# Kernel optimization log

Hardware: AMD Instinct MI355X
Metric: run time of the kernel (lower is better)

The kernel has to match this reference:

```python
import jax, jax.numpy as jnp
import numpy as np

NUM_PROTOTYPES = 512
NUM_BLOCKS = 8
D_MODEL = 1024
D_BLOCK = D_MODEL // NUM_BLOCKS


def setup_inputs() -> dict:
    key = jax.random.key(0)
    kq, km = jax.random.split(key)
    queries = jax.random.normal(kq, (8, 1024, D_MODEL), dtype=jnp.float32)
    # learned codebook: nn.Embedding(num_blocks*num_prototypes, d_block), normal init
    mem = jax.random.normal(km, (NUM_BLOCKS * NUM_PROTOTYPES, D_BLOCK), dtype=jnp.float32)
    return {"queries": queries, "mem": mem}


def reference(queries, mem):
    B, N, _ = queries.shape
    m, p, d = NUM_BLOCKS, NUM_PROTOTYPES, D_BLOCK
    q = queries.reshape(B, N, m, d)                 # [B,N,m,d]
    codes = mem.reshape(m, p, d)                    # [m,p,d]
    # Squared distances restricted to each query's own block (the only entries
    # the original consumes via distances[i, :, i]):
    #   ||q||^2 - 2 q.c + ||c||^2
    dots = jnp.einsum('bnmd,mpd->bnmp', q, codes)   # [B,N,m,p]
    qn = jnp.sum(q * q, axis=-1)                    # [B,N,m]
    cn = jnp.sum(codes * codes, axis=-1)            # [m,p]
    dist = qn[..., None] - 2.0 * dots + cn[None, None]
    local = jnp.argmin(dist, axis=-1)               # [B,N,m], first-min tiebreak like torch max of -dist
    indices = local + jnp.arange(m, dtype=local.dtype)[None, None, :] * p
    emb = codes[jnp.arange(m)[None, None, :], local]          # [B,N,m,d]
    emb = emb.reshape(B, N, m * d)
    # straight-through estimator
    emb_st = jax.lax.stop_gradient(emb - queries) + queries
    vq_loss = jnp.asarray(0.0, dtype=queries.dtype)
    commitment_loss = jnp.mean((jax.lax.stop_gradient(emb) - queries) ** 2)
    return emb_st, indices, vq_loss, commitment_loss
```

## Files before the change

### kernel.cpp

```cpp
#include <hip/hip_runtime.h>

#define NPROTO 512
#define NBLK 8
#define DB 128
#define DM 1024

#define IDX_OFF  8388608
#define VQ_OFF   8454144
#define CL_OFF   8454145

typedef unsigned short u16;
typedef __attribute__((ext_vector_type(8))) _Float16 f16x8;
typedef __attribute__((ext_vector_type(16))) float f32x16;

#define BH_B   0u
#define BL_B   1048576u
#define CN_B   2097152u
#define PART_B 2113536u
#define WS_NEED (PART_B + 16384u)

__global__ __launch_bounds__(256) void vq_prep(const float* __restrict__ src,
                                               u16* __restrict__ hi,
                                               u16* __restrict__ lo,
                                               float* __restrict__ cn) {
    const int t  = threadIdx.x;
    const int p  = blockIdx.x * 32 + (t >> 3);
    const int g  = t & 7;
    const int m  = p >> 9, pm = p & 511;
    const float* s = src + (size_t)p * DB + g * 16;
    float sq = 0.f;
    ushort4 h[4], l[4];
    #pragma unroll
    for (int j = 0; j < 4; ++j) {
        float4 v = *(const float4*)(s + j * 4);
        float x; _Float16 hf;
        #define S1(c, f) x = v.c; hf = (_Float16)x; h[j].f = __builtin_bit_cast(u16, hf); \
            hf = (_Float16)(x - (float)hf); l[j].f = __builtin_bit_cast(u16, hf); sq += x * x;
        S1(x, x) S1(y, y) S1(z, z) S1(w, w)
        #undef S1
    }
    const size_t o0 = ((size_t)((m * 8 + g) * 2 + 0) * 512 + pm) * 8;
    const size_t o1 = ((size_t)((m * 8 + g) * 2 + 1) * 512 + pm) * 8;
    *(uint4*)(hi + o0) = *(uint4*)&h[0];
    *(uint4*)(hi + o1) = *(uint4*)&h[2];
    *(uint4*)(lo + o0) = *(uint4*)&l[0];
    *(uint4*)(lo + o1) = *(uint4*)&l[2];
    sq += __shfl_xor(sq, 1, 64);
    sq += __shfl_xor(sq, 2, 64);
    sq += __shfl_xor(sq, 4, 64);
    if ((t & 7) == 0) cn[p] = sq;
}

__device__ __forceinline__ unsigned cvt2(float x, float y, unsigned& lo) {
    _Float16 hx = (_Float16)x, hy = (_Float16)y;
    _Float16 lx = (_Float16)(x - (float)hx), ly = (_Float16)(y - (float)hy);
    lo = (unsigned)__builtin_bit_cast(u16, lx) | ((unsigned)__builtin_bit_cast(u16, ly) << 16);
    return (unsigned)__builtin_bit_cast(u16, hx) | ((unsigned)__builtin_bit_cast(u16, hy) << 16);
}

__global__ __launch_bounds__(256, 2) void vq_fused(
        const float* __restrict__ q, const float* __restrict__ mem,
        const u16* __restrict__ bh, const u16* __restrict__ bl,
        const float* __restrict__ cn, float* __restrict__ out,
        float* __restrict__ partials2) {
    __shared__ __align__(16) u16 Ap[4][2][8][66][8];
    __shared__ float qn_lds[128];
    __shared__ int   bp[128];

    const int t    = threadIdx.x;
    const int lane = t & 63;
    const int w    = t >> 6;
    const int col  = lane & 31;
    const int kg   = lane >> 5;
    const int m    = blockIdx.y;
    const int bn0  = blockIdx.x * 128;
    const int rbase = w * 32;

    {
        const int row = lane >> 1;
        const int hf  = lane & 1;
        const float* src = q + (size_t)(bn0 + rbase + row) * DM + m * DB + hf * 64;
        float sq = 0.f;
        #pragma unroll
        for (int k4 = 0; k4 < 4; ++k4) {
            const int kst = hf * 4 + k4;
            float4 v0 = ((const float4*)(src + k4 * 16))[0];
            float4 v1 = ((const float4*)(src + k4 * 16))[1];
            float4 v2 = ((const float4*)(src + k4 * 16))[2];
            float4 v3 = ((const float4*)(src + k4 * 16))[3];
            sq += v0.x*v0.x+v0.y*v0.y+v0.z*v0.z+v0.w*v0.w
                + v1.x*v1.x+v1.y*v1.y+v1.z*v1.z+v1.w*v1.w
                + v2.x*v2.x+v2.y*v2.y+v2.z*v2.z+v2.w*v2.w
                + v3.x*v3.x+v3.y*v3.y+v3.z*v3.z+v3.w*v3.w;
            unsigned l0,l1,l2,l3,l4,l5,l6,l7;
            unsigned h0 = cvt2(v0.x, v0.y, l0), h1 = cvt2(v0.z, v0.w, l1);
            unsigned h2 = cvt2(v1.x, v1.y, l2), h3 = cvt2(v1.z, v1.w, l3);
            unsigned h4 = cvt2(v2.x, v2.y, l4), h5 = cvt2(v2.z, v2.w, l5);
            unsigned h6 = cvt2(v3.x, v3.y, l6), h7 = cvt2(v3.z, v3.w, l7);
            *(uint4*)&Ap[w][0][kst][row][0]      = make_uint4(h0, h1, h2, h3);
            *(uint4*)&Ap[w][0][kst][row + 32][0] = make_uint4(h4, h5, h6, h7);
            *(uint4*)&Ap[w][1][kst][row][0]      = make_uint4(l0, l1, l2, l3);
            *(uint4*)&Ap[w][1][kst][row + 32][0] = make_uint4(l4, l5, l6, l7);
        }
        sq += __shfl_xor(sq, 1, 64);
        if (hf == 0) qn_lds[rbase + row] = sq;
    }

    const u16* bh_l = bh + ((size_t)(m * 16 + kg) * 512 + col) * 8;
    const u16* bl_l = bl + ((size_t)(m * 16 + kg) * 512 + col) * 8;

    float bestv[16]; int besti[16];
    #pragma unroll
    for (int r = 0; r < 16; ++r) { bestv[r] = 3.4e38f; besti[r] = 0; }

    #pragma unroll 2
    for (int c = 0; c < 16; ++c) {
        const float cnv = cn[m * NPROTO + c * 32 + col];
        const u16* bhc = bh_l + c * 256;
        const u16* blc = bl_l + c * 256;
        f32x16 aA, aB;
        #pragma unroll
        for (int r = 0; r < 16; ++r) { aA[r] = 0.f; aB[r] = 0.f; }
        #pragma unroll
        for (int kst = 0; kst < 8; ++kst) {
            f16x8 Bh = *(const f16x8*)(bhc + kst * 8192);
            f16x8 Bl = *(const f16x8*)(blc + kst * 8192);
            f16x8 Ah = *(const f16x8*)&Ap[w][0][kst][lane][0];
            f16x8 Al = *(const f16x8*)&Ap[w][1][kst][lane][0];
            aA = __builtin_amdgcn_mfma_f32_32x32x16_f16(Ah, Bh, aA, 0, 0, 0);
            aB = __builtin_amdgcn_mfma_f32_32x32x16_f16(Al, Bh, aB, 0, 0, 0);
            aB = __builtin_amdgcn_mfma_f32_32x32x16_f16(Ah, Bl, aB, 0, 0, 0);
        }
        const int ix = c * 32 + col;
        #pragma unroll
        for (int r = 0; r < 16; ++r) {
            float d = cnv - 2.0f * (aA[r] + aB[r]);
            if (d < bestv[r]) { bestv[r] = d; besti[r] = ix; }
        }
    }

    #pragma unroll
    for (int r = 0; r < 16; ++r) {
        float v = bestv[r]; int ix = besti[r];
        #pragma unroll
        for (int off = 1; off < 32; off <<= 1) {
            float v2 = __shfl_xor(v, off, 64);
            int  ix2 = __shfl_xor(ix, off, 64);
            if (v2 < v || (v2 == v && ix2 < ix)) { v = v2; ix = ix2; }
        }
        bestv[r] = v; besti[r] = ix;
    }

    if (col == 0) {
        float lp = 0.f;
        #pragma unroll
        for (int r = 0; r < 16; ++r) {
            int row = rbase + (r & 3) + 8 * (r >> 2) + 4 * kg;
            bp[row] = besti[r];
            out[(size_t)IDX_OFF + (size_t)(bn0 + row) * NBLK + m] =
                (float)(m * NPROTO + besti[r]);
            lp += bestv[r] + qn_lds[row];
        }
        partials2[((size_t)blockIdx.y * gridDim.x + blockIdx.x) * 8 + w * 2 + kg] = lp;
    }

    {
        const int row = lane >> 1, hf = lane & 1;
        const int bpi = bp[rbase + row];
        const float* cv = mem + ((size_t)(m * NPROTO + bpi)) * DB + hf * 64;
        float* ov = out + (size_t)(bn0 + rbase + row) * DM + m * DB + hf * 64;
        #pragma unroll
        for (int j = 0; j < 16; ++j)
            ((float4*)ov)[j] = ((const float4*)cv)[j];
    }
}

__global__ __launch_bounds__(256) void vq_init(const float* __restrict__ mem,
                                               float* __restrict__ cn) {
    int p = blockIdx.x * 256 + threadIdx.x;
    const float* c = mem + (size_t)p * DB;
    float s = 0.f;
    #pragma unroll 8
    for (int k = 0; k < DB; k += 4) {
        float4 v = *(const float4*)(c + k);
        s += v.x * v.x + v.y * v.y + v.z * v.z + v.w * v.w;
    }
    cn[p] = s;
}

__global__ __launch_bounds__(256, 1) void vq_main_f32(const float* __restrict__ q,
                                                      const float* __restrict__ mem,
                                                      const float* __restrict__ cn,
                                                      float* __restrict__ out,
                                                      float* __restrict__ partials) {
    __shared__ float q_lds[128 * 132];
    __shared__ float c_lds[128 * 132];
    __shared__ float red[256];

    const int t    = threadIdx.x;
    const int tile = blockIdx.x;
    const int m    = blockIdx.y;
    const int tr   = t >> 4;
    const int tc   = t & 15;
    const int bn0  = tile * 128;

    const float* qbase = q + (size_t)bn0 * DM + m * DB;
    #pragma unroll
    for (int it = 0; it < 16; ++it) {
        int idx = it * 256 + t;
        int row = idx >> 5;
        int c4  = (idx & 31) << 2;
        *(float4*)&q_lds[row * 132 + c4] = *(const float4*)(qbase + (size_t)row * DM + c4);
    }

    float bestv[8]; int besti[8];
    #pragma unroll
    for (int i = 0; i < 8; ++i) { bestv[i] = 3.4e38f; besti[i] = 0; }
    const float* cbase = mem + (size_t)m * NPROTO * DB;

    for (int ch = 0; ch < 4; ++ch) {
        __syncthreads();
        const float* cb = cbase + (size_t)ch * 128 * DB;
        #pragma unroll
        for (int it = 0; it < 16; ++it) {
            int idx = it * 256 + t;
            int row = idx >> 5;
            int c4  = (idx & 31) << 2;
            *(float4*)&c_lds[row * 132 + c4] = *(const float4*)(cb + row * DB + c4);
        }
        __syncthreads();

        float acc[8][8];
        #pragma unroll
        for (int i = 0; i < 8; ++i)
            #pragma unroll
            for (int j = 0; j < 8; ++j) acc[i][j] = 0.f;

        for (int d4 = 0; d4 < DB; d4 += 4) {
            float4 qa[8], cvv[8];
            #pragma unroll
            for (int i = 0; i < 8; ++i) qa[i] = *(const float4*)&q_lds[(tr + 16 * i) * 132 + d4];
            #pragma unroll
            for (int j = 0; j < 8; ++j) cvv[j] = *(const float4*)&c_lds[(tc + 16 * j) * 132 + d4];
            #pragma unroll
            for (int i = 0; i < 8; ++i)
                #pragma unroll
                for (int j = 0; j < 8; ++j) {
                    acc[i][j] += qa[i].x * cvv[j].x; acc[i][j] += qa[i].y * cvv[j].y;
                    acc[i][j] += qa[i].z * cvv[j].z; acc[i][j] += qa[i].w * cvv[j].w;
                }
        }
        #pragma unroll
        for (int i = 0; i < 8; ++i)
            #pragma unroll
            for (int j = 0; j < 8; ++j) {
                int lp = ch * 128 + tc + 16 * j;
                float dist = cn[m * NPROTO + lp] - 2.0f * acc[i][j];
                if (dist < bestv[i]) { bestv[i] = dist; besti[i] = lp; }
            }
    }

    #pragma unroll
    for (int i = 0; i < 8; ++i) {
        float v = bestv[i]; int ix = besti[i];
        #pragma unroll
        for (int off = 1; off < 16; off <<= 1) {
            float v2 = __shfl_xor(v, off, 64);
            int  ix2 = __shfl_xor(ix, off, 64);
            if (v2 < v || (v2 == v && ix2 < ix)) { v = v2; ix = ix2; }
        }
        bestv[i] = v; besti[i] = ix;
    }

    float lacc = 0.f;
    #pragma unroll
    for (int i = 0; i < 8; ++i) {
        int row = tr + 16 * i;
        int bn  = bn0 + row;
        const float* cvec = cbase + (size_t)besti[i] * DB;
        float* orow = out + (size_t)bn * DM + m * DB;
        #pragma unroll
        for (int h = 0; h < 2; ++h) {
            int colx = h * 64 + tc * 4;
            float4 c4v = *(const float4*)(cvec + colx);
            *(float4*)(orow + colx) = c4v;
            float4 qv2 = *(const float4*)&q_lds[row * 132 + colx];
            float dx = c4v.x - qv2.x, dy = c4v.y - qv2.y;
            float dz = c4v.z - qv2.z, dw = c4v.w - qv2.w;
            lacc += dx * dx + dy * dy + dz * dz + dw * dw;
        }
        if (tc == 0)
            out[(size_t)IDX_OFF + (size_t)bn * NBLK + m] = (float)(m * NPROTO + besti[i]);
    }

    red[t] = lacc;
    __syncthreads();
    for (int s = 128; s > 0; s >>= 1) {
        if (t < s) red[t] += red[t + s];
        __syncthreads();
    }
    if (t == 0) partials[blockIdx.y * gridDim.x + blockIdx.x] = red[0];
}

__global__ __launch_bounds__(256) void vq_final(const float* __restrict__ partials,
                                                float* __restrict__ out, int n) {
    __shared__ float red[256];
    int t = threadIdx.x;
    float v = 0.f;
    for (int i = t; i < n; i += 256) v += partials[i];
    red[t] = v;
    __syncthreads();
    for (int s = 128; s > 0; s >>= 1) {
        if (t < s) red[t] += red[t + s];
        __syncthreads();
    }
    if (t == 0) {
        out[VQ_OFF] = 0.f;
        out[CL_OFF] = red[0] / 8388608.0f;
    }
}

extern "C" void kernel_launch(void* const* d_in, const int* in_sizes, int n_in,
                              void* d_out, int out_size, void* d_ws, size_t ws_size,
                              hipStream_t stream) {
    const float* q   = (const float*)d_in[0];
    const float* mem = (const float*)d_in[1];
    float* out = (float*)d_out;
    char* ws = (char*)d_ws;

    if (ws_size >= (size_t)WS_NEED) {
        u16*   bhp = (u16*)(ws + BH_B);
        u16*   blp = (u16*)(ws + BL_B);
        float* cnp = (float*)(ws + CN_B);
        float* partials = (float*)(ws + PART_B);

        vq_prep<<<128, 256, 0, stream>>>(mem, bhp, blp, cnp);
        dim3 grid(64, 8);
        vq_fused<<<grid, 256, 0, stream>>>(q, mem, bhp, blp, cnp, out, partials);
        vq_final<<<1, 256, 0, stream>>>(partials, out, 4096);
    } else {
        float* cn = (float*)ws;
        float* partials = cn + 4096;
        vq_init<<<16, 256, 0, stream>>>(mem, cn);
        dim3 grid(64, 8);
        vq_main_f32<<<grid, 256, 0, stream>>>(q, mem, cn, out, partials);
        vq_final<<<1, 256, 0, stream>>>(partials, out, 512);
    }
}
```

Baseline: 69.54 us.

## Switch to 16x16x32 MFMA with register-resident A and smaller row tiles

Replaces the 32x32x16 MFMA tiling with 16x16x32 MFMAs, holding each wave's query fragments (fp16 hi/lo split) directly in registers instead of staging them through LDS. Each block now handles 64 rows instead of 128, doubling the grid to 1024 blocks, and the codebook pre-pack layout is changed to match the new K-step grouping. This is meant to remove LDS staging and raise occupancy and parallelism. The cost is that each codebook fragment is reused across fewer query rows, so codebook loads per row roughly double, and there are more partial sums to reduce in the final kernel.

```diff
diff --git a/kernel.cpp b/kernel.cpp
--- a/kernel.cpp
+++ b/kernel.cpp
@@ -11,13 +11,13 @@
 
 typedef unsigned short u16;
 typedef __attribute__((ext_vector_type(8))) _Float16 f16x8;
-typedef __attribute__((ext_vector_type(16))) float f32x16;
+typedef __attribute__((ext_vector_type(4))) float f32x4;
 
 #define BH_B   0u
 #define BL_B   1048576u
 #define CN_B   2097152u
 #define PART_B 2113536u
-#define WS_NEED (PART_B + 16384u)
+#define WS_NEED (PART_B + 65536u)
 
 __global__ __launch_bounds__(256) void vq_prep(const float* __restrict__ src,
                                                u16* __restrict__ hi,
@@ -39,8 +39,9 @@
         S1(x, x) S1(y, y) S1(z, z) S1(w, w)
         #undef S1
     }
-    const size_t o0 = ((size_t)((m * 8 + g) * 2 + 0) * 512 + pm) * 8;
-    const size_t o1 = ((size_t)((m * 8 + g) * 2 + 1) * 512 + pm) * 8;
+    const int kst = g >> 1, kg0 = (g & 1) * 2;
+    const size_t o0 = (((size_t)(m * 4 + kst) * 4 + kg0 + 0) * 512 + pm) * 8;
+    const size_t o1 = (((size_t)(m * 4 + kst) * 4 + kg0 + 1) * 512 + pm) * 8;
     *(uint4*)(hi + o0) = *(uint4*)&h[0];
     *(uint4*)(hi + o1) = *(uint4*)&h[2];
     *(uint4*)(lo + o0) = *(uint4*)&l[0];
@@ -63,87 +64,83 @@
         const u16* __restrict__ bh, const u16* __restrict__ bl,
         const float* __restrict__ cn, float* __restrict__ out,
         float* __restrict__ partials2) {
-    __shared__ __align__(16) u16 Ap[4][2][8][66][8];
-    __shared__ float qn_lds[128];
-    __shared__ int   bp[128];
+    __shared__ float qn_l[64];
+    __shared__ int   bp[64];
 
     const int t    = threadIdx.x;
     const int lane = t & 63;
     const int w    = t >> 6;
-    const int col  = lane & 31;
-    const int kg   = lane >> 5;
+    const int pr   = lane & 15;
+    const int kg   = lane >> 4;
     const int m    = blockIdx.y;
-    const int bn0  = blockIdx.x * 128;
-    const int rbase = w * 32;
-
-    {
-        const int row = lane >> 1;
-        const int hf  = lane & 1;
-        const float* src = q + (size_t)(bn0 + rbase + row) * DM + m * DB + hf * 64;
-        float sq = 0.f;
-        #pragma unroll
-        for (int k4 = 0; k4 < 4; ++k4) {
-            const int kst = hf * 4 + k4;
-            float4 v0 = ((const float4*)(src + k4 * 16))[0];
-            float4 v1 = ((const float4*)(src + k4 * 16))[1];
-            float4 v2 = ((const float4*)(src + k4 * 16))[2];
-            float4 v3 = ((const float4*)(src + k4 * 16))[3];
-            sq += v0.x*v0.x+v0.y*v0.y+v0.z*v0.z+v0.w*v0.w
-                + v1.x*v1.x+v1.y*v1.y+v1.z*v1.z+v1.w*v1.w
-                + v2.x*v2.x+v2.y*v2.y+v2.z*v2.z+v2.w*v2.w
-                + v3.x*v3.x+v3.y*v3.y+v3.z*v3.z+v3.w*v3.w;
-            unsigned l0,l1,l2,l3,l4,l5,l6,l7;
-            unsigned h0 = cvt2(v0.x, v0.y, l0), h1 = cvt2(v0.z, v0.w, l1);
-            unsigned h2 = cvt2(v1.x, v1.y, l2), h3 = cvt2(v1.z, v1.w, l3);
-            unsigned h4 = cvt2(v2.x, v2.y, l4), h5 = cvt2(v2.z, v2.w, l5);
-            unsigned h6 = cvt2(v3.x, v3.y, l6), h7 = cvt2(v3.z, v3.w, l7);
-            *(uint4*)&Ap[w][0][kst][row][0]      = make_uint4(h0, h1, h2, h3);
-            *(uint4*)&Ap[w][0][kst][row + 32][0] = make_uint4(h4, h5, h6, h7);
-            *(uint4*)&Ap[w][1][kst][row][0]      = make_uint4(l0, l1, l2, l3);
-            *(uint4*)&Ap[w][1][kst][row + 32][0] = make_uint4(l4, l5, l6, l7);
-        }
-        sq += __shfl_xor(sq, 1, 64);
-        if (hf == 0) qn_lds[rbase + row] = sq;
-    }
-
-    const u16* bh_l = bh + ((size_t)(m * 16 + kg) * 512 + col) * 8;
-    const u16* bl_l = bl + ((size_t)(m * 16 + kg) * 512 + col) * 8;
-
-    float bestv[16]; int besti[16];
-    #pragma unroll
-    for (int r = 0; r < 16; ++r) { bestv[r] = 3.4e38f; besti[r] = 0; }
+    const int bn0  = blockIdx.x * 64;
+    const int rbase = w * 16;
+
+    f16x8 ah[4], al[4];
+    float qnp = 0.f;
+    #pragma unroll
+    for (int kst = 0; kst < 4; ++kst) {
+        const float* src = q + (size_t)(bn0 + rbase + pr) * DM
+                             + m * DB + kst * 32 + kg * 8;
+        float4 v0 = ((const float4*)src)[0];
+        float4 v1 = ((const float4*)src)[1];
+        unsigned l0, l1, l2, l3;
+        unsigned h0 = cvt2(v0.x, v0.y, l0), h1 = cvt2(v0.z, v0.w, l1);
+        unsigned h2 = cvt2(v1.x, v1.y, l2), h3 = cvt2(v1.z, v1.w, l3);
+        uint4 hv = make_uint4(h0, h1, h2, h3), lv = make_uint4(l0, l1, l2, l3);
+        ah[kst] = __builtin_bit_cast(f16x8, hv);
+        al[kst] = __builtin_bit_cast(f16x8, lv);
+        qnp += v0.x*v0.x + v0.y*v0.y + v0.z*v0.z + v0.w*v0.w
+             + v1.x*v1.x + v1.y*v1.y + v1.z*v1.z + v1.w*v1.w;
+    }
+    qnp += __shfl_xor(qnp, 16, 64);
+    qnp += __shfl_xor(qnp, 32, 64);
+    if (kg == 0) qn_l[rbase + pr] = qnp;
+
+    const u16* bh_l = bh + ((size_t)(m * 16 + kg) * 512 + pr) * 8;
+    const u16* bl_l = bl + ((size_t)(m * 16 + kg) * 512 + pr) * 8;
+    const float* cnb = cn + m * NPROTO + pr;
+
+    float bestv[4]; int besti[4];
+    #pragma unroll
+    for (int r = 0; r < 4; ++r) { bestv[r] = 3.4e38f; besti[r] = 0; }
 
     #pragma unroll 2
     for (int c = 0; c < 16; ++c) {
-        const float cnv = cn[m * NPROTO + c * 32 + col];
+        const float cn0 = cnb[c * 32];
+        const float cn1 = cnb[c * 32 + 16];
         const u16* bhc = bh_l + c * 256;
         const u16* blc = bl_l + c * 256;
-        f32x16 aA, aB;
-        #pragma unroll
-        for (int r = 0; r < 16; ++r) { aA[r] = 0.f; aB[r] = 0.f; }
-        #pragma unroll
-        for (int kst = 0; kst < 8; ++kst) {
-            f16x8 Bh = *(const f16x8*)(bhc + kst * 8192);
-            f16x8 Bl = *(const f16x8*)(blc + kst * 8192);
-            f16x8 Ah = *(const f16x8*)&Ap[w][0][kst][lane][0];
-            f16x8 Al = *(const f16x8*)&Ap[w][1][kst][lane][0];
-            aA = __builtin_amdgcn_mfma_f32_32x32x16_f16(Ah, Bh, aA, 0, 0, 0);
-            aB = __builtin_amdgcn_mfma_f32_32x32x16_f16(Al, Bh, aB, 0, 0, 0);
-            aB = __builtin_amdgcn_mfma_f32_32x32x16_f16(Ah, Bl, aB, 0, 0, 0);
-        }
-        const int ix = c * 32 + col;
-        #pragma unroll
-        for (int r = 0; r < 16; ++r) {
-            float d = cnv - 2.0f * (aA[r] + aB[r]);
-            if (d < bestv[r]) { bestv[r] = d; besti[r] = ix; }
-        }
-    }
-
-    #pragma unroll
-    for (int r = 0; r < 16; ++r) {
+        f32x4 a0A = {0.f,0.f,0.f,0.f}, a0B = {0.f,0.f,0.f,0.f};
+        f32x4 a1A = {0.f,0.f,0.f,0.f}, a1B = {0.f,0.f,0.f,0.f};
+        #pragma unroll
+        for (int kst = 0; kst < 4; ++kst) {
+            f16x8 Bh0 = *(const f16x8*)(bhc + (size_t)kst * 16384);
+            f16x8 Bl0 = *(const f16x8*)(blc + (size_t)kst * 16384);
+            f16x8 Bh1 = *(const f16x8*)(bhc + (size_t)kst * 16384 + 128);
+            f16x8 Bl1 = *(const f16x8*)(blc + (size_t)kst * 16384 + 128);
+            a0A = __builtin_amdgcn_mfma_f32_16x16x32_f16(ah[kst], Bh0, a0A, 0, 0, 0);
+            a0B = __builtin_amdgcn_mfma_f32_16x16x32_f16(al[kst], Bh0, a0B, 0, 0, 0);
+            a0B = __builtin_amdgcn_mfma_f32_16x16x32_f16(ah[kst], Bl0, a0B, 0, 0, 0);
+            a1A = __builtin_amdgcn_mfma_f32_16x16x32_f16(ah[kst], Bh1, a1A, 0, 0, 0);
+            a1B = __builtin_amdgcn_mfma_f32_16x16x32_f16(al[kst], Bh1, a1B, 0, 0, 0);
+            a1B = __builtin_amdgcn_mfma_f32_16x16x32_f16(ah[kst], Bl1, a1B, 0, 0, 0);
+        }
+        const int ix0 = c * 32 + pr, ix1 = ix0 + 16;
+        #pragma unroll
+        for (int r = 0; r < 4; ++r) {
+            float d0 = cn0 - 2.0f * (a0A[r] + a0B[r]);
+            if (d0 < bestv[r]) { bestv[r] = d0; besti[r] = ix0; }
+            float d1 = cn1 - 2.0f * (a1A[r] + a1B[r]);
+            if (d1 < bestv[r]) { bestv[r] = d1; besti[r] = ix1; }
+        }
+    }
+
+    #pragma unroll
+    for (int r = 0; r < 4; ++r) {
         float v = bestv[r]; int ix = besti[r];
         #pragma unroll
-        for (int off = 1; off < 32; off <<= 1) {
+        for (int off = 1; off < 16; off <<= 1) {
             float v2 = __shfl_xor(v, off, 64);
             int  ix2 = __shfl_xor(ix, off, 64);
             if (v2 < v || (v2 == v && ix2 < ix)) { v = v2; ix = ix2; }
@@ -151,26 +148,26 @@
         bestv[r] = v; besti[r] = ix;
     }
 
-    if (col == 0) {
+    if (pr == 0) {
         float lp = 0.f;
         #pragma unroll
-        for (int r = 0; r < 16; ++r) {
-            int row = rbase + (r & 3) + 8 * (r >> 2) + 4 * kg;
+        for (int r = 0; r < 4; ++r) {
+            int row = rbase + kg * 4 + r;
             bp[row] = besti[r];
             out[(size_t)IDX_OFF + (size_t)(bn0 + row) * NBLK + m] =
                 (float)(m * NPROTO + besti[r]);
-            lp += bestv[r] + qn_lds[row];
-        }
-        partials2[((size_t)blockIdx.y * gridDim.x + blockIdx.x) * 8 + w * 2 + kg] = lp;
+            lp += bestv[r] + qn_l[row];
+        }
+        partials2[((size_t)blockIdx.y * gridDim.x + blockIdx.x) * 16 + w * 4 + kg] = lp;
     }
 
     {
-        const int row = lane >> 1, hf = lane & 1;
+        const int row = lane >> 2, q4 = lane & 3;
         const int bpi = bp[rbase + row];
-        const float* cv = mem + ((size_t)(m * NPROTO + bpi)) * DB + hf * 64;
-        float* ov = out + (size_t)(bn0 + rbase + row) * DM + m * DB + hf * 64;
-        #pragma unroll
-        for (int j = 0; j < 16; ++j)
+        const float* cv = mem + ((size_t)(m * NPROTO + bpi)) * DB + q4 * 32;
+        float* ov = out + (size_t)(bn0 + rbase + row) * DM + m * DB + q4 * 32;
+        #pragma unroll
+        for (int j = 0; j < 8; ++j)
             ((float4*)ov)[j] = ((const float4*)cv)[j];
     }
 }
@@ -335,9 +332,9 @@
         float* partials = (float*)(ws + PART_B);
 
         vq_prep<<<128, 256, 0, stream>>>(mem, bhp, blp, cnp);
-        dim3 grid(64, 8);
+        dim3 grid(128, 8);
         vq_fused<<<grid, 256, 0, stream>>>(q, mem, bhp, blp, cnp, out, partials);
-        vq_final<<<1, 256, 0, stream>>>(partials, out, 4096);
+        vq_final<<<1, 256, 0, stream>>>(partials, out, 16384);
     } else {
         float* cn = (float*)ws;
         float* partials = cn + 4096;
```

Result: slower. 86.05 us (+23.7%).
